# Optimization experiments

Hardware: AMD Instinct MI355X
Metric: run time of the kernel (lower is better)

The kernel has to match this reference:

```python
import jax, jax.numpy as jnp
import numpy as np

B, T, C = 2, 2048, 1024
N_HEAD, N_GROUP = 16, 4
N_KV = N_HEAD // N_GROUP          # 4
HEAD_DIM = C // N_HEAD            # 64
ROPE_BASE = 10000.0
INIT_STD = 0.02


def setup_inputs() -> dict:
    key = jax.random.key(0)
    ks = jax.random.split(key, 5)
    kvC = N_KV * HEAD_DIM
    return {
        "x": jax.random.normal(ks[0], (B, T, C), jnp.float32),
        "w_q": jax.random.normal(ks[1], (C, C), jnp.float32) * INIT_STD,
        "b_q": jnp.zeros((C,), jnp.float32),
        "w_k": jax.random.normal(ks[2], (C, kvC), jnp.float32) * INIT_STD,
        "b_k": jnp.zeros((kvC,), jnp.float32),
        "w_v": jax.random.normal(ks[3], (C, kvC), jnp.float32) * INIT_STD,
        "b_v": jnp.zeros((kvC,), jnp.float32),
        "w_o": jax.random.normal(ks[4], (C, C), jnp.float32) * INIT_STD,
        "b_o": jnp.zeros((C,), jnp.float32),
    }


def reference(x, w_q, b_q, w_k, b_k, w_v, b_v, w_o, b_o):
    Bx, Tx, Cx = x.shape
    # projections (torch Linear math with weights stored as [in, out])
    q = (x @ w_q + b_q).reshape(Bx, Tx, N_HEAD, HEAD_DIM).transpose(0, 2, 1, 3)  # [B,H,T,hd]
    k = (x @ w_k + b_k).reshape(Bx, Tx, N_KV, HEAD_DIM).transpose(0, 2, 1, 3)    # [B,KV,T,hd]
    v = (x @ w_v + b_v).reshape(Bx, Tx, N_KV, HEAD_DIM).transpose(0, 2, 1, 3)

    # RoPE with INTERLEAVED pair convention: pairs are (dim 2i, dim 2i+1)
    inv_freq = 1.0 / (ROPE_BASE ** (jnp.arange(0, HEAD_DIM, 2, dtype=jnp.float32) / HEAD_DIM))
    freqs = jnp.arange(Tx, dtype=jnp.float32)[:, None] * inv_freq[None, :]       # [T, hd/2]
    cos, sin = jnp.cos(freqs), jnp.sin(freqs)

    def rope(t):
        tp = t.reshape(*t.shape[:-1], HEAD_DIM // 2, 2)
        e, o = tp[..., 0], tp[..., 1]          # even/odd lanes, [B,h,T,hd/2]
        er = e * cos - o * sin
        orr = e * sin + o * cos
        return jnp.stack([er, orr], axis=-1).reshape(t.shape)

    q, k = rope(q), rope(k)

    # GQA: duplicate each KV head n_group times (consecutively, like repeat_interleave)
    k = jnp.repeat(k, N_GROUP, axis=1)   # [B,H,T,hd]
    v = jnp.repeat(v, N_GROUP, axis=1)

    attn = jnp.einsum('bhqd,bhkd->bhqk', q, k) / np.sqrt(HEAD_DIM).astype(np.float32)
    causal = jnp.tril(jnp.ones((Tx, Tx), bool))
    attn = jnp.where(causal, attn, -jnp.inf)
    attn = jax.nn.softmax(attn, axis=-1)

    out = jnp.einsum('bhqk,bhkd->bhqd', attn, v)            # [B,H,T,hd]
    out = out.transpose(0, 2, 1, 3).reshape(Bx, Tx, Cx)
    return out @ w_o + b_o
```

## Files before the change

### kernel.cpp

```cpp
#include <hip/hip_runtime.h>
#include <hip/hip_bf16.h>

typedef __hip_bfloat16 bf16;
typedef __attribute__((ext_vector_type(8))) short short8_t;
typedef __attribute__((ext_vector_type(4))) short short4_t;
typedef __attribute__((ext_vector_type(4))) float f32x4;

#define B_SZ   2
#define T_SEQ  2048
#define C_DIM  1024
#define NH     16
#define NKV    4
#define HD     64
#define QKVW   1536
#define MTOK   (B_SZ * T_SEQ)

#define LOG2_BASE_OVER_32 0.4152410118609203f
#define Q_SCALE 0.1803368801111204f

__device__ __forceinline__ short f2bs(float f) {
    unsigned u = __float_as_uint(f);
    u += 0x7FFFu + ((u >> 16) & 1u);
    return (short)(u >> 16);
}
__device__ __forceinline__ short f2bs_trunc(float f) {
    return (short)(__float_as_uint(f) >> 16);
}
__device__ __forceinline__ float bs2f(short s) {
    unsigned u = ((unsigned)(unsigned short)s) << 16;
    return __uint_as_float(u);
}
__device__ __forceinline__ float dpp_xor1(float x) {
    return __int_as_float(
        __builtin_amdgcn_update_dpp(0, __float_as_int(x), 0xB1, 0xF, 0xF, true));
}

__device__ __forceinline__ void transpose_tile(
    const float* __restrict__ W, short* __restrict__ Wt,
    int K, int N, int n0, int k0, int tid)
{
    __shared__ float tile[32][33];
    int tx = tid & 31, ty = tid >> 5;
    #pragma unroll
    for (int i = 0; i < 4; ++i)
        tile[ty + 8 * i][tx] = W[(size_t)(k0 + ty + 8 * i) * N + n0 + tx];
    __syncthreads();
    #pragma unroll
    for (int i = 0; i < 4; ++i)
        Wt[(size_t)(n0 + ty + 8 * i) * K + k0 + tx] = f2bs(tile[tx][ty + 8 * i]);
}

__global__ __launch_bounds__(256) void prep_kernel(
    const float* __restrict__ x,
    const float* __restrict__ w_q, const float* __restrict__ w_k,
    const float* __restrict__ w_v, const float* __restrict__ w_o,
    const float* __restrict__ b_q, const float* __restrict__ b_k,
    const float* __restrict__ b_v,
    short* __restrict__ Xb, short* __restrict__ Wqkv, short* __restrict__ Wto,
    float* __restrict__ Bqkv, float2* __restrict__ Tab)
{
    int blk = blockIdx.x, tid = threadIdx.x;
    if (blk < 4096) {
        int i = blk * 1024 + tid * 4;
        float4 v = *(const float4*)(x + i);
        short4_t o;
        o[0] = f2bs(v.x); o[1] = f2bs(v.y); o[2] = f2bs(v.z); o[3] = f2bs(v.w);
        *(short4_t*)(Xb + i) = o;
    } else if (blk < 5120) {
        int l = blk - 4096;
        transpose_tile(w_q, Wqkv, C_DIM, C_DIM, (l & 31) * 32, (l >> 5) * 32, tid);
    } else if (blk < 5376) {
        int l = blk - 5120;
        transpose_tile(w_k, Wqkv + (size_t)1024 * C_DIM, C_DIM, 256,
                       (l & 7) * 32, (l >> 3) * 32, tid);
    } else if (blk < 5632) {
        int l = blk - 5376;
        transpose_tile(w_v, Wqkv + (size_t)1280 * C_DIM, C_DIM, 256,
                       (l & 7) * 32, (l >> 3) * 32, tid);
    } else if (blk < 6656) {
        int l = blk - 5632;
        transpose_tile(w_o, Wto, C_DIM, C_DIM, (l & 31) * 32, (l >> 5) * 32, tid);
    } else if (blk < 6662) {
        int i = (blk - 6656) * 256 + tid;
        float v;
        if (i < 1024)      v = b_q[i];
        else if (i < 1280) v = b_k[i - 1024];
        else               v = b_v[i - 1280];
        Bqkv[i] = v;
    } else {
        int idx = (blk - 6662) * 256 + tid;
        int t = idx >> 5, i = idx & 31;
        float ang = (float)t * exp2f(-(float)i * LOG2_BASE_OVER_32);
        Tab[idx] = make_float2(cosf(ang), sinf(ang));
    }
}

__global__ __launch_bounds__(256) void gemm_qkv(
    const short* __restrict__ A, const short* __restrict__ Bt,
    const float* __restrict__ bias, const float2* __restrict__ Tab,
    short* __restrict__ QKVb, short* __restrict__ Vt)
{
    __shared__ __align__(16) short smem[15360];
    short (*sA)[128][40] = (short(*)[128][40])smem;
    short (*sB)[64][40]  = (short(*)[64][40])(smem + 10240);

    const int K = C_DIM;
    int m0 = blockIdx.y * 128;
    int n0 = blockIdx.x * 64;
    int tid  = threadIdx.x;
    int w    = tid >> 6, lane = tid & 63;
    int quad = lane >> 4, l16 = lane & 15;
    int wm = w & 1, wn = w >> 1;

    f32x4 acc[4][2] = {};

    short8_t ra[2], rb;
    #pragma unroll
    for (int it = 0; it < 2; ++it) {
        int slot = tid + 256 * it, row = slot >> 2, g = (slot & 3) * 8;
        ra[it] = *(const short8_t*)(A + (size_t)(m0 + row) * K + g);
    }
    {
        int row = tid >> 2, g = (tid & 3) * 8;
        rb = *(const short8_t*)(Bt + (size_t)(n0 + row) * K + g);
    }

    int buf = 0;
    for (int k0 = 0; k0 < K; k0 += 32, buf ^= 1) {
        #pragma unroll
        for (int it = 0; it < 2; ++it) {
            int slot = tid + 256 * it, row = slot >> 2, g = (slot & 3) * 8;
            *(short8_t*)&sA[buf][row][g] = ra[it];
        }
        {
            int row = tid >> 2, g = (tid & 3) * 8;
            *(short8_t*)&sB[buf][row][g] = rb;
        }
        if (k0 + 32 < K) {
            #pragma unroll
            for (int it = 0; it < 2; ++it) {
                int slot = tid + 256 * it, row = slot >> 2, g = (slot & 3) * 8;
                ra[it] = *(const short8_t*)(A + (size_t)(m0 + row) * K + k0 + 32 + g);
            }
            int row = tid >> 2, g = (tid & 3) * 8;
            rb = *(const short8_t*)(Bt + (size_t)(n0 + row) * K + k0 + 32 + g);
        }
        __syncthreads();

        short8_t af[4], bfr[2];
        #pragma unroll
        for (int mt = 0; mt < 4; ++mt)
            af[mt] = *(const short8_t*)&sA[buf][wm * 64 + mt * 16 + l16][quad * 8];
        #pragma unroll
        for (int nt = 0; nt < 2; ++nt)
            bfr[nt] = *(const short8_t*)&sB[buf][wn * 32 + nt * 16 + l16][quad * 8];
        #pragma unroll
        for (int mt = 0; mt < 4; ++mt)
            #pragma unroll
            for (int nt = 0; nt < 2; ++nt)
                acc[mt][nt] = __builtin_amdgcn_mfma_f32_16x16x32_bf16(
                    af[mt], bfr[nt], acc[mt][nt], 0, 0, 0);
    }

    if (n0 < 1280) {
        float scale = (n0 < 1024) ? Q_SCALE : 1.0f;
        float sgn   = (l16 & 1) ? 1.0f : -1.0f;
        #pragma unroll
        for (int nt = 0; nt < 2; ++nt) {
            int col = n0 + wn * 32 + nt * 16 + l16;
            int ip  = (col & 63) >> 1;
            float bv = bias[col];
            #pragma unroll
            for (int mt = 0; mt < 4; ++mt) {
                #pragma unroll
                for (int r = 0; r < 4; ++r) {
                    int row = m0 + wm * 64 + mt * 16 + quad * 4 + r;
                    float v = acc[mt][nt][r] + bv;
                    float po = dpp_xor1(v);
                    float2 cs = Tab[(row & (T_SEQ - 1)) * 32 + ip];
                    float res = (v * cs.x + sgn * po * cs.y) * scale;
                    QKVb[(size_t)row * QKVW + col] = f2bs(res);
                }
            }
        }
    } else {
        __syncthreads();
        short (*sT)[136] = (short(*)[136])smem;
        #pragma unroll
        for (int nt = 0; nt < 2; ++nt) {
            int col_l = wn * 32 + nt * 16 + l16;
            float bv = bias[n0 + col_l];
            #pragma unroll
            for (int mt = 0; mt < 4; ++mt)
                #pragma unroll
                for (int r = 0; r < 4; ++r)
                    sT[col_l][wm * 64 + mt * 16 + quad * 4 + r] =
                        f2bs(acc[mt][nt][r] + bv);
        }
        __syncthreads();
        int d0 = n0 - 1280;
        #pragma unroll
        for (int it = 0; it < 4; ++it) {
            int slot = tid + 256 * it;
            int dl = slot >> 4, seg = (slot & 15) * 8;
            *(short8_t*)(Vt + (size_t)(d0 + dl) * MTOK + m0 + seg) =
                *(const short8_t*)&sT[dl][seg];
        }
    }
}

__global__ __launch_bounds__(256) void gemm_mfma_o(
    const short* __restrict__ A, const short* __restrict__ Bt,
    const float* __restrict__ bias, float* __restrict__ C,
    int M, int N, int K)
{
    __shared__ __align__(16) short smem[15360];
    short (*sA)[128][40] = (short(*)[128][40])smem;
    short (*sB)[64][40]  = (short(*)[64][40])(smem + 10240);

    int m0 = blockIdx.y * 128;
    int n0 = blockIdx.x * 64;
    int tid  = threadIdx.x;
    int w    = tid >> 6, lane = tid & 63;
    int quad = lane >> 4, l16 = lane & 15;
    int wm = w & 1, wn = w >> 1;

    f32x4 acc[4][2] = {};

    short8_t ra[2], rb;
    #pragma unroll
    for (int it = 0; it < 2; ++it) {
        int slot = tid + 256 * it, row = slot >> 2, g = (slot & 3) * 8;
        ra[it] = *(const short8_t*)(A + (size_t)(m0 + row) * K + g);
    }
    {
        int row = tid >> 2, g = (tid & 3) * 8;
        rb = *(const short8_t*)(Bt + (size_t)(n0 + row) * K + g);
    }

    int buf = 0;
    for (int k0 = 0; k0 < K; k0 += 32, buf ^= 1) {
        #pragma unroll
        for (int it = 0; it < 2; ++it) {
            int slot = tid + 256 * it, row = slot >> 2, g = (slot & 3) * 8;
            *(short8_t*)&sA[buf][row][g] = ra[it];
        }
        {
            int row = tid >> 2, g = (tid & 3) * 8;
            *(short8_t*)&sB[buf][row][g] = rb;
        }
        if (k0 + 32 < K) {
            #pragma unroll
            for (int it = 0; it < 2; ++it) {
                int slot = tid + 256 * it, row = slot >> 2, g = (slot & 3) * 8;
                ra[it] = *(const short8_t*)(A + (size_t)(m0 + row) * K + k0 + 32 + g);
            }
            int row = tid >> 2, g = (tid & 3) * 8;
            rb = *(const short8_t*)(Bt + (size_t)(n0 + row) * K + k0 + 32 + g);
        }
        __syncthreads();

        short8_t af[4], bfr[2];
        #pragma unroll
        for (int mt = 0; mt < 4; ++mt)
            af[mt] = *(const short8_t*)&sA[buf][wm * 64 + mt * 16 + l16][quad * 8];
        #pragma unroll
        for (int nt = 0; nt < 2; ++nt)
            bfr[nt] = *(const short8_t*)&sB[buf][wn * 32 + nt * 16 + l16][quad * 8];
        #pragma unroll
        for (int mt = 0; mt < 4; ++mt)
            #pragma unroll
            for (int nt = 0; nt < 2; ++nt)
                acc[mt][nt] = __builtin_amdgcn_mfma_f32_16x16x32_bf16(
                    af[mt], bfr[nt], acc[mt][nt], 0, 0, 0);
    }

    #pragma unroll
    for (int mt = 0; mt < 4; ++mt) {
        #pragma unroll
        for (int nt = 0; nt < 2; ++nt) {
            int col = n0 + wn * 32 + nt * 16 + l16;
            float bv = bias[col];
            #pragma unroll
            for (int r = 0; r < 4; ++r) {
                int row = m0 + wm * 64 + mt * 16 + quad * 4 + r;
                C[(size_t)row * N + col] = acc[mt][nt][r] + bv;
            }
        }
    }
}

__global__ __launch_bounds__(256) void attn_mfma11(
    const short* __restrict__ QKV, const short* __restrict__ Vt,
    short* __restrict__ Op0, short* __restrict__ Op1,
    float* __restrict__ Mp, float* __restrict__ Lp)
{
    __shared__ __align__(16) short sK [64][72];
    __shared__ __align__(16) short sVt[64][72];
    __shared__ __align__(16) short sP [4][16][72];

    const int tid  = threadIdx.x;
    const int w    = tid >> 6;
    const int lane = tid & 63;
    const int quad = lane >> 4;
    const int l16  = lane & 15;

    int blk = blockIdx.x;
    int grp = blk & 7;
    int s   = (blk >> 3) & 1;
    int tq  = 127 - (blk >> 4);
    int kvh = grp & 3;
    int b   = grp >> 2;
    int h   = kvh * 4 + w;
    int ct  = tq >> 2;
    int tg  = tq * 16 + l16;

    const short* qptr = QKV + ((size_t)(b * T_SEQ) + tg) * QKVW + h * HD;
    short8_t qf0 = *(const short8_t*)(qptr + quad * 8);
    short8_t qf1 = *(const short8_t*)(qptr + quad * 8 + 32);

    const short* kbase  = QKV + (size_t)b * T_SEQ * QKVW + 1024 + kvh * HD;
    const short* vtbase = Vt + (size_t)(kvh * HD) * MTOK + b * T_SEQ;

    float m_l = -INFINITY, l_l = 0.f;
    f32x4 oacc[4];
    #pragma unroll
    for (int dt = 0; dt < 4; ++dt) oacc[dt] = (f32x4){0.f, 0.f, 0.f, 0.f};

    const int kkey = tid >> 3, kd = (tid & 7) * 8;
    const int vdim = tid >> 3, vseg = (tid & 7) * 8;

    short8_t kr[2], vr[2];
    {
        int j0 = s * 64;
        #pragma unroll
        for (int it = 0; it < 2; ++it) {
            kr[it] = *(const short8_t*)(kbase + (size_t)(j0 + kkey + 32 * it) * QKVW + kd);
            vr[it] = *(const short8_t*)(vtbase + (size_t)(vdim + 32 * it) * MTOK + j0 + vseg);
        }
    }

    for (int c = s; c <= ct; c += 2) {
        __syncthreads();
        #pragma unroll
        for (int it = 0; it < 2; ++it) {
            *(short8_t*)&sK [kkey + 32 * it][kd]   = kr[it];
            *(short8_t*)&sVt[vdim + 32 * it][vseg] = vr[it];
        }
        __syncthreads();
        if (c + 2 <= ct) {
            int jn = (c + 2) * 64;
            #pragma unroll
            for (int it = 0; it < 2; ++it) {
                kr[it] = *(const short8_t*)(kbase + (size_t)(jn + kkey + 32 * it) * QKVW + kd);
                vr[it] = *(const short8_t*)(vtbase + (size_t)(vdim + 32 * it) * MTOK + jn + vseg);
            }
        }

        f32x4 sacc[4];
        #pragma unroll
        for (int kt = 0; kt < 4; ++kt) {
            f32x4 z = {0.f, 0.f, 0.f, 0.f};
            short8_t kf0 = *(const short8_t*)&sK[l16 + 16 * kt][quad * 8];
            short8_t kf1 = *(const short8_t*)&sK[l16 + 16 * kt][quad * 8 + 32];
            z = __builtin_amdgcn_mfma_f32_16x16x32_bf16(kf0, qf0, z, 0, 0, 0);
            z = __builtin_amdgcn_mfma_f32_16x16x32_bf16(kf1, qf1, z, 0, 0, 0);
            sacc[kt] = z;
        }

        if (c == ct) {
            int j0 = c * 64;
            #pragma unroll
            for (int kt = 0; kt < 4; ++kt)
                #pragma unroll
                for (int r = 0; r < 4; ++r)
                    if (j0 + 16 * kt + quad * 4 + r > tg) sacc[kt][r] = -INFINITY;
        }

        float vmax = sacc[0][0];
        #pragma unroll
        for (int kt = 0; kt < 4; ++kt)
            #pragma unroll
            for (int r = 0; r < 4; ++r) vmax = fmaxf(vmax, sacc[kt][r]);
        vmax = fmaxf(vmax, __shfl_xor(vmax, 16));
        vmax = fmaxf(vmax, __shfl_xor(vmax, 32));
        float mnew = fmaxf(m_l, vmax);
        float al = exp2f(m_l - mnew);
        m_l = mnew;

        float psum = 0.f;
        #pragma unroll
        for (int kt = 0; kt < 4; ++kt) {
            short4_t pk;
            #pragma unroll
            for (int r = 0; r < 4; ++r) {
                float p = exp2f(sacc[kt][r] - mnew);
                psum += p;
                pk[r] = f2bs_trunc(p);
            }
            *(short4_t*)&sP[w][l16][16 * kt + 4 * quad] = pk;
        }
        psum += __shfl_xor(psum, 16);
        psum += __shfl_xor(psum, 32);
        l_l = l_l * al + psum;

        if (__any(al < 1.f)) {
            #pragma unroll
            for (int r = 0; r < 4; ++r) {
                float alr = __shfl(al, quad * 4 + r);
                #pragma unroll
                for (int dt = 0; dt < 4; ++dt) oacc[dt][r] *= alr;
            }
        }

        short8_t pf0 = *(const short8_t*)&sP[w][l16][quad * 8];
        short8_t pf1 = *(const short8_t*)&sP[w][l16][quad * 8 + 32];
        #pragma unroll
        for (int dt = 0; dt < 4; ++dt) {
            short8_t vf0 = *(const short8_t*)&sVt[16 * dt + l16][quad * 8];
            short8_t vf1 = *(const short8_t*)&sVt[16 * dt + l16][quad * 8 + 32];
            oacc[dt] = __builtin_amdgcn_mfma_f32_16x16x32_bf16(pf0, vf0, oacc[dt], 0, 0, 0);
            oacc[dt] = __builtin_amdgcn_mfma_f32_16x16x32_bf16(pf1, vf1, oacc[dt], 0, 0, 0);
        }
    }

    int tix = (b * NH + h) * 128 + tq;
    if (quad == 0) {
        Mp[(size_t)(s * 4096 + tix) * 16 + l16] = m_l;
        Lp[(size_t)(s * 4096 + tix) * 16 + l16] = l_l;
    }
    short* Op = s ? Op1 : Op0;
    #pragma unroll
    for (int r = 0; r < 4; ++r) {
        int q = quad * 4 + r;
        #pragma unroll
        for (int dt = 0; dt < 4; ++dt)
            Op[(size_t)tix * 1024 + q * 64 + 16 * dt + l16] = f2bs(oacc[dt][r]);
    }
}

__global__ __launch_bounds__(256) void attn_combine(
    const short* __restrict__ Op0, const short* __restrict__ Op1,
    const float* __restrict__ Mp, const float* __restrict__ Lp,
    short* __restrict__ Ab)
{
    int blk = blockIdx.x;
    int tid = threadIdx.x;
    int q = tid >> 4, d0 = (tid & 15) * 4;
    int tq = blk & 127, bh = blk >> 7, h = bh & 15, b = bh >> 4;

    float m0 = Mp[(size_t)blk * 16 + q];
    float m1 = Mp[(size_t)(4096 + blk) * 16 + q];
    float l0 = Lp[(size_t)blk * 16 + q];
    float l1 = Lp[(size_t)(4096 + blk) * 16 + q];
    float ms = fmaxf(m0, m1);
    float a0 = exp2f(m0 - ms), a1 = exp2f(m1 - ms);
    float inv = __builtin_amdgcn_rcpf(l0 * a0 + l1 * a1);

    short4_t o0 = *(const short4_t*)&Op0[(size_t)blk * 1024 + q * 64 + d0];
    short4_t o1 = *(const short4_t*)&Op1[(size_t)blk * 1024 + q * 64 + d0];
    short4_t res;
    #pragma unroll
    for (int i = 0; i < 4; ++i)
        res[i] = f2bs((bs2f(o0[i]) * a0 + bs2f(o1[i]) * a1) * inv);
    *(short4_t*)&Ab[((size_t)(b * T_SEQ + tq * 16 + q)) * C_DIM + h * HD + d0] = res;
}

extern "C" void kernel_launch(void* const* d_in, const int* in_sizes, int n_in,
                              void* d_out, int out_size, void* d_ws, size_t ws_size,
                              hipStream_t stream)
{
    const float* x   = (const float*)d_in[0];
    const float* w_q = (const float*)d_in[1];
    const float* b_q = (const float*)d_in[2];
    const float* w_k = (const float*)d_in[3];
    const float* b_k = (const float*)d_in[4];
    const float* w_v = (const float*)d_in[5];
    const float* b_v = (const float*)d_in[6];
    const float* w_o = (const float*)d_in[7];
    const float* b_o = (const float*)d_in[8];
    float* out = (float*)d_out;

    char* ws = (char*)d_ws;
    short*  Xb   = (short*) (ws);
    short*  Ab   = (short*) (ws + ((size_t)8  << 20));
    short*  QKVb = (short*) (ws + ((size_t)16 << 20));
    short*  Wqkv = (short*) (ws + ((size_t)28 << 20));
    short*  Wto  = (short*) (ws + ((size_t)31 << 20));
    float*  Bqkv = (float*) (ws + ((size_t)33 << 20));
    float2* Tab  = (float2*)(ws + ((size_t)33 << 20) + 8192);
    short*  Vt   = (short*) (ws + ((size_t)34 << 20));
    short*  Op0  = Xb;
    short*  Op1  = (short*) (ws + ((size_t)36 << 20));
    float*  Mp   = (float*) (ws + ((size_t)44 << 20));
    float*  Lp   = (float*) (ws + ((size_t)44 << 20) + (1 << 19));

    const int M = MTOK;

    prep_kernel<<<6918, 256, 0, stream>>>(
        x, w_q, w_k, w_v, w_o, b_q, b_k, b_v, Xb, Wqkv, Wto, Bqkv, Tab);

    gemm_qkv<<<dim3(QKVW / 64, M / 128), 256, 0, stream>>>(
        Xb, Wqkv, Bqkv, Tab, QKVb, Vt);

    attn_mfma11<<<2048, 256, 0, stream>>>(QKVb, Vt, Op0, Op1, Mp, Lp);

    attn_combine<<<4096, 256, 0, stream>>>(Op0, Op1, Mp, Lp, Ab);

    gemm_mfma_o<<<dim3(C_DIM / 64, M / 128), 256, 0, stream>>>(
        Ab, Wto, b_o, out, M, C_DIM, C_DIM);
}
```

Before: 179.3 us.

## Load GEMM tiles directly into LDS with global_load_lds in projection kernels

Both projection GEMMs (QKV and output) now fetch their A and B tiles with global_load_lds, which writes from global memory straight into LDS and bypasses the register staging. The LDS layout becomes unpadded and single-buffered, and a second barrier per k-step is added. The register prefetch that overlapped the next tile's load with the MFMA work is removed. The aim is lower VGPR use and fewer LDS store instructions, at the cost of no load/compute overlap and possible LDS bank conflicts on the unpadded rows.

Result: slower. 185.6 us (+3.5%).

```diff
diff --git a/kernel.cpp b/kernel.cpp
--- a/kernel.cpp
+++ b/kernel.cpp
@@ -33,6 +33,11 @@
 __device__ __forceinline__ float dpp_xor1(float x) {
     return __int_as_float(
         __builtin_amdgcn_update_dpp(0, __float_as_int(x), 0xB1, 0xF, 0xF, true));
+}
+__device__ __forceinline__ void gl_lds16(const short* g, short* l) {
+    __builtin_amdgcn_global_load_lds(
+        (const __attribute__((address_space(1))) void*)g,
+        (__attribute__((address_space(3))) void*)l, 16, 0, 0);
 }
 
 __device__ __forceinline__ void transpose_tile(
@@ -100,9 +105,9 @@
     const float* __restrict__ bias, const float2* __restrict__ Tab,
     short* __restrict__ QKVb, short* __restrict__ Vt)
 {
-    __shared__ __align__(16) short smem[15360];
-    short (*sA)[128][40] = (short(*)[128][40])smem;
-    short (*sB)[64][40]  = (short(*)[64][40])(smem + 10240);
+    __shared__ __align__(16) short smem[8704];
+    short* sA = smem;
+    short* sB = smem + 4096;
 
     const int K = C_DIM;
     int m0 = blockIdx.y * 128;
@@ -112,54 +117,38 @@
     int quad = lane >> 4, l16 = lane & 15;
     int wm = w & 1, wn = w >> 1;
 
+    int aflat0 = (w * 2 + 0) * 64 + lane;
+    int aflat1 = (w * 2 + 1) * 64 + lane;
+    const short* agp0 = A + (size_t)(m0 + (aflat0 >> 2)) * K + (aflat0 & 3) * 8;
+    const short* agp1 = A + (size_t)(m0 + (aflat1 >> 2)) * K + (aflat1 & 3) * 8;
+    int bflat = w * 64 + lane;
+    const short* bgp = Bt + (size_t)(n0 + (bflat >> 2)) * K + (bflat & 3) * 8;
+    short* al0 = sA + (w * 2 + 0) * 512;
+    short* al1 = sA + (w * 2 + 1) * 512;
+    short* bl  = sB + w * 512;
+
     f32x4 acc[4][2] = {};
 
-    short8_t ra[2], rb;
-    #pragma unroll
-    for (int it = 0; it < 2; ++it) {
-        int slot = tid + 256 * it, row = slot >> 2, g = (slot & 3) * 8;
-        ra[it] = *(const short8_t*)(A + (size_t)(m0 + row) * K + g);
-    }
-    {
-        int row = tid >> 2, g = (tid & 3) * 8;
-        rb = *(const short8_t*)(Bt + (size_t)(n0 + row) * K + g);
-    }
-
-    int buf = 0;
-    for (int k0 = 0; k0 < K; k0 += 32, buf ^= 1) {
-        #pragma unroll
-        for (int it = 0; it < 2; ++it) {
-            int slot = tid + 256 * it, row = slot >> 2, g = (slot & 3) * 8;
-            *(short8_t*)&sA[buf][row][g] = ra[it];
-        }
-        {
-            int row = tid >> 2, g = (tid & 3) * 8;
-            *(short8_t*)&sB[buf][row][g] = rb;
-        }
-        if (k0 + 32 < K) {
-            #pragma unroll
-            for (int it = 0; it < 2; ++it) {
-                int slot = tid + 256 * it, row = slot >> 2, g = (slot & 3) * 8;
-                ra[it] = *(const short8_t*)(A + (size_t)(m0 + row) * K + k0 + 32 + g);
-            }
-            int row = tid >> 2, g = (tid & 3) * 8;
-            rb = *(const short8_t*)(Bt + (size_t)(n0 + row) * K + k0 + 32 + g);
-        }
+    for (int k0 = 0; k0 < K; k0 += 32) {
+        gl_lds16(agp0 + k0, al0);
+        gl_lds16(agp1 + k0, al1);
+        gl_lds16(bgp + k0, bl);
         __syncthreads();
 
         short8_t af[4], bfr[2];
         #pragma unroll
         for (int mt = 0; mt < 4; ++mt)
-            af[mt] = *(const short8_t*)&sA[buf][wm * 64 + mt * 16 + l16][quad * 8];
+            af[mt] = *(const short8_t*)&sA[(wm * 64 + mt * 16 + l16) * 32 + quad * 8];
         #pragma unroll
         for (int nt = 0; nt < 2; ++nt)
-            bfr[nt] = *(const short8_t*)&sB[buf][wn * 32 + nt * 16 + l16][quad * 8];
+            bfr[nt] = *(const short8_t*)&sB[(wn * 32 + nt * 16 + l16) * 32 + quad * 8];
         #pragma unroll
         for (int mt = 0; mt < 4; ++mt)
             #pragma unroll
             for (int nt = 0; nt < 2; ++nt)
                 acc[mt][nt] = __builtin_amdgcn_mfma_f32_16x16x32_bf16(
                     af[mt], bfr[nt], acc[mt][nt], 0, 0, 0);
+        __syncthreads();
     }
 
     if (n0 < 1280) {
@@ -184,7 +173,6 @@
             }
         }
     } else {
-        __syncthreads();
         short (*sT)[136] = (short(*)[136])smem;
         #pragma unroll
         for (int nt = 0; nt < 2; ++nt) {
@@ -214,9 +202,9 @@
     const float* __restrict__ bias, float* __restrict__ C,
     int M, int N, int K)
 {
-    __shared__ __align__(16) short smem[15360];
-    short (*sA)[128][40] = (short(*)[128][40])smem;
-    short (*sB)[64][40]  = (short(*)[64][40])(smem + 10240);
+    __shared__ __align__(16) short smem[6144];
+    short* sA = smem;
+    short* sB = smem + 4096;
 
     int m0 = blockIdx.y * 128;
     int n0 = blockIdx.x * 64;
@@ -225,54 +213,38 @@
     int quad = lane >> 4, l16 = lane & 15;
     int wm = w & 1, wn = w >> 1;
 
+    int aflat0 = (w * 2 + 0) * 64 + lane;
+    int aflat1 = (w * 2 + 1) * 64 + lane;
+    const short* agp0 = A + (size_t)(m0 + (aflat0 >> 2)) * K + (aflat0 & 3) * 8;
+    const short* agp1 = A + (size_t)(m0 + (aflat1 >> 2)) * K + (aflat1 & 3) * 8;
+    int bflat = w * 64 + lane;
+    const short* bgp = Bt + (size_t)(n0 + (bflat >> 2)) * K + (bflat & 3) * 8;
+    short* al0 = sA + (w * 2 + 0) * 512;
+    short* al1 = sA + (w * 2 + 1) * 512;
+    short* bl  = sB + w * 512;
+
     f32x4 acc[4][2] = {};
 
-    short8_t ra[2], rb;
-    #pragma unroll
-    for (int it = 0; it < 2; ++it) {
-        int slot = tid + 256 * it, row = slot >> 2, g = (slot & 3) * 8;
-        ra[it] = *(const short8_t*)(A + (size_t)(m0 + row) * K + g);
-    }
-    {
-        int row = tid >> 2, g = (tid & 3) * 8;
-        rb = *(const short8_t*)(Bt + (size_t)(n0 + row) * K + g);
-    }
-
-    int buf = 0;
-    for (int k0 = 0; k0 < K; k0 += 32, buf ^= 1) {
-        #pragma unroll
-        for (int it = 0; it < 2; ++it) {
-            int slot = tid + 256 * it, row = slot >> 2, g = (slot & 3) * 8;
-            *(short8_t*)&sA[buf][row][g] = ra[it];
-        }
-        {
-            int row = tid >> 2, g = (tid & 3) * 8;
-            *(short8_t*)&sB[buf][row][g] = rb;
-        }
-        if (k0 + 32 < K) {
-            #pragma unroll
-            for (int it = 0; it < 2; ++it) {
-                int slot = tid + 256 * it, row = slot >> 2, g = (slot & 3) * 8;
-                ra[it] = *(const short8_t*)(A + (size_t)(m0 + row) * K + k0 + 32 + g);
-            }
-            int row = tid >> 2, g = (tid & 3) * 8;
-            rb = *(const short8_t*)(Bt + (size_t)(n0 + row) * K + k0 + 32 + g);
-        }
+    for (int k0 = 0; k0 < K; k0 += 32) {
+        gl_lds16(agp0 + k0, al0);
+        gl_lds16(agp1 + k0, al1);
+        gl_lds16(bgp + k0, bl);
         __syncthreads();
 
         short8_t af[4], bfr[2];
         #pragma unroll
         for (int mt = 0; mt < 4; ++mt)
-            af[mt] = *(const short8_t*)&sA[buf][wm * 64 + mt * 16 + l16][quad * 8];
+            af[mt] = *(const short8_t*)&sA[(wm * 64 + mt * 16 + l16) * 32 + quad * 8];
         #pragma unroll
         for (int nt = 0; nt < 2; ++nt)
-            bfr[nt] = *(const short8_t*)&sB[buf][wn * 32 + nt * 16 + l16][quad * 8];
+            bfr[nt] = *(const short8_t*)&sB[(wn * 32 + nt * 16 + l16) * 32 + quad * 8];
         #pragma unroll
         for (int mt = 0; mt < 4; ++mt)
             #pragma unroll
             for (int nt = 0; nt < 2; ++nt)
                 acc[mt][nt] = __builtin_amdgcn_mfma_f32_16x16x32_bf16(
                     af[mt], bfr[nt], acc[mt][nt], 0, 0, 0);
+        __syncthreads();
     }
 
     #pragma unroll
```
